# Performance work log

Hardware: AMD Instinct MI355X
Metric: run time of the kernel (lower is better)

The kernel has to match this reference:

```python
import jax, jax.numpy as jnp
import numpy as np

N = 50000
E = 800000
D = 128
L = 2


def setup_inputs() -> dict:
    key = jax.random.key(0)
    ks = jax.random.split(key, 8)
    x = jax.random.normal(ks[0], (N, D), dtype=jnp.float32)
    edge_index = jax.random.randint(ks[1], (2, E), 0, N, dtype=jnp.int64)
    s = 1.0 / np.sqrt(D)
    Wl = jax.random.uniform(ks[2], (L, D, D), jnp.float32, -s, s)  # neighbor transform (with bias)
    bl = jax.random.uniform(ks[3], (L, D), jnp.float32, -s, s)
    Wr = jax.random.uniform(ks[4], (L, D, D), jnp.float32, -s, s)  # root/self transform (no bias)
    W = jax.random.uniform(ks[5], (D, D), jnp.float32, -s, s)      # final Linear
    b = jax.random.uniform(ks[6], (D,), jnp.float32, -s, s)
    return {"x": x, "edge_index": edge_index, "Wl": Wl, "bl": bl, "Wr": Wr, "W": W, "b": b}


def reference(x, edge_index, Wl, bl, Wr, W, b):
    src, dst = edge_index[0], edge_index[1]
    n = x.shape[0]
    for l in range(Wl.shape[0]):
        # gather neighbor (source) features, scatter-max into destination nodes
        agg = jax.ops.segment_max(x[src], dst, num_segments=n)  # [N, D]
        agg = jnp.where(jnp.isneginf(agg), 0.0, agg)  # PyG: isolated nodes -> 0
        # SAGEConv: lin_l(agg) + lin_r(x)
        x = agg @ Wl[l].T + bl[l] + x @ Wr[l].T
        x = jax.nn.relu(x)
    return x @ W.T + b
```

## Files before the change

kernel.cpp:

```cpp
#include <hip/hip_runtime.h>
#include <math.h>

#define NN 50000
#define NE 800000
#define DD 128
#define NBUCK 196
#define PTILE 4096
#define PBLOCKS 196

typedef unsigned short u16;
typedef short s8v __attribute__((ext_vector_type(8)));
typedef float f16v __attribute__((ext_vector_type(16)));

__device__ __forceinline__ u16 f2bf(float f) {
    unsigned u = __float_as_uint(f);
    return (u16)((u + 0x7FFFu + ((u >> 16) & 1u)) >> 16);
}
__device__ __forceinline__ float bf2f(u16 h) {
    return __uint_as_float(((unsigned)h) << 16);
}
__device__ __forceinline__ float bflo(unsigned u) { return __uint_as_float(u << 16); }
__device__ __forceinline__ float bfhi(unsigned u) { return __uint_as_float(u & 0xFFFF0000u); }

__global__ __launch_bounds__(256) void zero_int(int* __restrict__ p, int n) {
    int i = blockIdx.x * 256 + threadIdx.x;
    if (i < n) p[i] = 0;
}

__global__ __launch_bounds__(256) void bucket_hist(const int* __restrict__ ei,
                                                   int* __restrict__ bcnt) {
    __shared__ int h[NBUCK];
    for (int i = threadIdx.x; i < NBUCK; i += 256) h[i] = 0;
    __syncthreads();
    int e0 = blockIdx.x * PTILE;
#pragma unroll
    for (int i = 0; i < 16; i++) {
        int e = e0 + i * 256 + threadIdx.x;
        if (e < NE) atomicAdd(&h[ei[NE + e] >> 8], 1);
    }
    __syncthreads();
    for (int i = threadIdx.x; i < NBUCK; i += 256)
        if (h[i]) atomicAdd(&bcnt[i], h[i]);
}

__global__ __launch_bounds__(256) void bucket_scan(const int* __restrict__ bcnt,
                                                   int* __restrict__ bbase,
                                                   int* __restrict__ bcur,
                                                   int* __restrict__ rowptr) {
    __shared__ int s[256];
    int t = threadIdx.x;
    int v = (t < NBUCK) ? bcnt[t] : 0;
    s[t] = v;
    __syncthreads();
    for (int o = 1; o < 256; o <<= 1) {
        int u = (t >= o) ? s[t - o] : 0;
        __syncthreads();
        s[t] += u;
        __syncthreads();
    }
    int ex = s[t] - v;
    if (t < NBUCK) { bbase[t] = ex; bcur[t] = ex; }
    if (t == 0) rowptr[NN] = NE;
}

__global__ __launch_bounds__(256) void bucket_partition(const int* __restrict__ ei,
                                                        int* __restrict__ bcur,
                                                        unsigned* __restrict__ packed) {
    __shared__ int h[NBUCK];
    __shared__ int base[NBUCK];
    int t = threadIdx.x;
    for (int i = t; i < NBUCK; i += 256) h[i] = 0;
    __syncthreads();
    int e0 = blockIdx.x * PTILE;
    int dsts[16], srcs[16];
#pragma unroll
    for (int i = 0; i < 16; i++) {
        int e = e0 + i * 256 + t;
        if (e < NE) {
            dsts[i] = ei[NE + e];
            srcs[i] = ei[e];
            atomicAdd(&h[dsts[i] >> 8], 1);
        } else dsts[i] = -1;
    }
    __syncthreads();
    for (int i = t; i < NBUCK; i += 256) {
        int c = h[i];
        base[i] = c ? atomicAdd(&bcur[i], c) : 0;
    }
    __syncthreads();
    for (int i = t; i < NBUCK; i += 256) h[i] = 0;
    __syncthreads();
#pragma unroll
    for (int i = 0; i < 16; i++) {
        if (dsts[i] >= 0) {
            int bk = dsts[i] >> 8;
            int r = atomicAdd(&h[bk], 1);
            packed[base[bk] + r] = (unsigned)srcs[i] | ((unsigned)(dsts[i] & 255) << 16);
        }
    }
}

__global__ __launch_bounds__(256) void bucket_csr(const unsigned* __restrict__ packed,
                                                  const int* __restrict__ bcnt,
                                                  const int* __restrict__ bbase,
                                                  int* __restrict__ rowptr,
                                                  int* __restrict__ col) {
    __shared__ int deg[256];
    __shared__ int off[256];
    int bk = blockIdx.x;
    int cnt = bcnt[bk], base = bbase[bk];
    int t = threadIdx.x;
    deg[t] = 0;
    __syncthreads();
    for (int i = t; i < cnt; i += 256) atomicAdd(&deg[packed[base + i] >> 16], 1);
    __syncthreads();
    int v = deg[t];
    off[t] = v;
    __syncthreads();
    for (int o = 1; o < 256; o <<= 1) {
        int u = (t >= o) ? off[t - o] : 0;
        __syncthreads();
        off[t] += u;
        __syncthreads();
    }
    int ex = off[t] - v;
    int node = (bk << 8) + t;
    if (node < NN) rowptr[node] = base + ex;
    deg[t] = ex;
    __syncthreads();
    for (int i = t; i < cnt; i += 256) {
        unsigned p = packed[base + i];
        int dl = p >> 16;
        int r = atomicAdd(&deg[dl], 1);
        col[base + r] = (int)(p & 0xFFFFu);
    }
}

__global__ __launch_bounds__(256) void conv_bf16(const float4* __restrict__ in,
                                                 ushort4* __restrict__ out, int n4) {
    int i = blockIdx.x * 256 + threadIdx.x;
    if (i >= n4) return;
    float4 v = in[i];
    ushort4 o;
    o.x = f2bf(v.x); o.y = f2bf(v.y); o.z = f2bf(v.z); o.w = f2bf(v.w);
    out[i] = o;
}

template<int NKC16, bool TWO>
__global__ __launch_bounds__(256) void pack_weights(const float* __restrict__ Wl,
                                                    const float* __restrict__ Wr,
                                                    u16* __restrict__ out) {
    int o = blockIdx.x * 256 + threadIdx.x;
    if (o >= NKC16 * 2048) return;
    int j = o & 7;
    int l = (o >> 3) & 63;
    int cn = o >> 9;
    int n = cn & 3;
    int c = cn >> 2;
    int colj = n * 32 + (l & 31);
    int k = c * 16 + (l >> 5) * 8 + j;
    float v;
    if (TWO) v = (k < DD) ? Wl[colj * DD + k] : Wr[colj * DD + (k - DD)];
    else     v = Wl[colj * DD + k];
    out[o] = f2bf(v);
}

__global__ __launch_bounds__(256) void agg_kernel_bf(const uint4* __restrict__ xb4,
                                                     const int* __restrict__ row_ptr,
                                                     const int* __restrict__ col,
                                                     uint4* __restrict__ aggb4) {
    int node = blockIdx.x * 16 + (threadIdx.x >> 4);
    if (node >= NN) return;
    int j = threadIdx.x & 15;
    int s0 = row_ptr[node], s1 = row_ptr[node + 1];
    if (s0 == s1) {
        aggb4[(size_t)node * 16 + j] = make_uint4(0, 0, 0, 0);
        return;
    }
    float m0[8], m1[8], m2[8], m3[8];
#pragma unroll
    for (int q = 0; q < 8; q++) { m0[q] = m1[q] = m2[q] = m3[q] = -INFINITY; }
    int i = s0;
    for (; i + 4 <= s1; i += 4) {
        int c0 = col[i], c1 = col[i + 1], c2 = col[i + 2], c3 = col[i + 3];
        uint4 v0 = xb4[(size_t)c0 * 16 + j];
        uint4 v1 = xb4[(size_t)c1 * 16 + j];
        uint4 v2 = xb4[(size_t)c2 * 16 + j];
        uint4 v3 = xb4[(size_t)c3 * 16 + j];
        m0[0] = fmaxf(m0[0], bflo(v0.x)); m0[1] = fmaxf(m0[1], bfhi(v0.x));
        m0[2] = fmaxf(m0[2], bflo(v0.y)); m0[3] = fmaxf(m0[3], bfhi(v0.y));
        m0[4] = fmaxf(m0[4], bflo(v0.z)); m0[5] = fmaxf(m0[5], bfhi(v0.z));
        m0[6] = fmaxf(m0[6], bflo(v0.w)); m0[7] = fmaxf(m0[7], bfhi(v0.w));
        m1[0] = fmaxf(m1[0], bflo(v1.x)); m1[1] = fmaxf(m1[1], bfhi(v1.x));
        m1[2] = fmaxf(m1[2], bflo(v1.y)); m1[3] = fmaxf(m1[3], bfhi(v1.y));
        m1[4] = fmaxf(m1[4], bflo(v1.z)); m1[5] = fmaxf(m1[5], bfhi(v1.z));
        m1[6] = fmaxf(m1[6], bflo(v1.w)); m1[7] = fmaxf(m1[7], bfhi(v1.w));
        m2[0] = fmaxf(m2[0], bflo(v2.x)); m2[1] = fmaxf(m2[1], bfhi(v2.x));
        m2[2] = fmaxf(m2[2], bflo(v2.y)); m2[3] = fmaxf(m2[3], bfhi(v2.y));
        m2[4] = fmaxf(m2[4], bflo(v2.z)); m2[5] = fmaxf(m2[5], bfhi(v2.z));
        m2[6] = fmaxf(m2[6], bflo(v2.w)); m2[7] = fmaxf(m2[7], bfhi(v2.w));
        m3[0] = fmaxf(m3[0], bflo(v3.x)); m3[1] = fmaxf(m3[1], bfhi(v3.x));
        m3[2] = fmaxf(m3[2], bflo(v3.y)); m3[3] = fmaxf(m3[3], bfhi(v3.y));
        m3[4] = fmaxf(m3[4], bflo(v3.z)); m3[5] = fmaxf(m3[5], bfhi(v3.z));
        m3[6] = fmaxf(m3[6], bflo(v3.w)); m3[7] = fmaxf(m3[7], bfhi(v3.w));
    }
    for (; i < s1; i++) {
        uint4 v = xb4[(size_t)col[i] * 16 + j];
        m0[0] = fmaxf(m0[0], bflo(v.x)); m0[1] = fmaxf(m0[1], bfhi(v.x));
        m0[2] = fmaxf(m0[2], bflo(v.y)); m0[3] = fmaxf(m0[3], bfhi(v.y));
        m0[4] = fmaxf(m0[4], bflo(v.z)); m0[5] = fmaxf(m0[5], bfhi(v.z));
        m0[6] = fmaxf(m0[6], bflo(v.w)); m0[7] = fmaxf(m0[7], bfhi(v.w));
    }
#pragma unroll
    for (int q = 0; q < 8; q++) m0[q] = fmaxf(fmaxf(m0[q], m1[q]), fmaxf(m2[q], m3[q]));
    uint4 o;
    o.x = (__float_as_uint(m0[0]) >> 16) | (__float_as_uint(m0[1]) & 0xFFFF0000u);
    o.y = (__float_as_uint(m0[2]) >> 16) | (__float_as_uint(m0[3]) & 0xFFFF0000u);
    o.z = (__float_as_uint(m0[4]) >> 16) | (__float_as_uint(m0[5]) & 0xFFFF0000u);
    o.w = (__float_as_uint(m0[6]) >> 16) | (__float_as_uint(m0[7]) & 0xFFFF0000u);
    aggb4[(size_t)node * 16 + j] = o;
}

template<int NKC16, bool TWO_SRC, bool RELU, bool OUT_BF16>
__global__ __launch_bounds__(256) void mfma_gemm(const u16* __restrict__ srcA,
                                                 const u16* __restrict__ srcB,
                                                 const u16* __restrict__ Bpk,
                                                 const float* __restrict__ bias,
                                                 void* __restrict__ outv) {
    __shared__ s8v ldsB[NKC16 * 4 * 64];
    int tid = threadIdx.x;
#pragma unroll
    for (int i = 0; i < NKC16; i++) {
        ((float4*)ldsB)[tid + 256 * i] = ((const float4*)Bpk)[tid + 256 * i];
    }

    int wt = tid >> 6;
    int lane = tid & 63;
    int row0 = blockIdx.x * 128 + wt * 32;
    int rload = row0 + (lane & 31);
    if (rload > NN - 1) rload = NN - 1;
    int koff = (lane >> 5) * 8;

    f16v acc[4];
#pragma unroll
    for (int n = 0; n < 4; n++) acc[n] = (f16v)(0.0f);

    __syncthreads();

#pragma unroll
    for (int c = 0; c < NKC16; c++) {
        const u16* s = srcA;
        int kk = c * 16;
        if (TWO_SRC && c >= 8) { s = srcB; kk = (c - 8) * 16; }
        s8v a = *(const s8v*)(s + (size_t)rload * DD + kk + koff);
#pragma unroll
        for (int n = 0; n < 4; n++) {
            s8v b = ldsB[(c * 4 + n) * 64 + lane];
            acc[n] = __builtin_amdgcn_mfma_f32_32x32x16_bf16(a, b, acc[n], 0, 0, 0);
        }
    }

    int rowadd = 4 * (lane >> 5);
#pragma unroll
    for (int n = 0; n < 4; n++) {
        int colj = n * 32 + (lane & 31);
        float bj = bias[colj];
#pragma unroll
        for (int r = 0; r < 16; r++) {
            int row = row0 + (r & 3) + 8 * (r >> 2) + rowadd;
            if (row < NN) {
                float v = acc[n][r] + bj;
                if (RELU) v = fmaxf(v, 0.0f);
                if (OUT_BF16) ((u16*)outv)[(size_t)row * DD + colj] = f2bf(v);
                else          ((float*)outv)[(size_t)row * DD + colj] = v;
            }
        }
    }
}

extern "C" void kernel_launch(void* const* d_in, const int* in_sizes, int n_in,
                              void* d_out, int out_size, void* d_ws, size_t ws_size,
                              hipStream_t stream) {
    const float* x  = (const float*)d_in[0];
    const int*   ei = (const int*)d_in[1];
    const float* Wl = (const float*)d_in[2];
    const float* bl = (const float*)d_in[3];
    const float* Wr = (const float*)d_in[4];
    const float* W  = (const float*)d_in[5];
    const float* b  = (const float*)d_in[6];
    float* out = (float*)d_out;

    u16* aggb = (u16*)d_ws;
    u16* hb0  = aggb + (size_t)NN * DD;
    u16* hb1  = hb0 + (size_t)NN * DD;
    u16* Bpk0 = hb1 + (size_t)NN * DD;
    u16* Bpk1 = Bpk0 + 32768;
    u16* Bpkf = Bpk1 + 32768;
    unsigned* packed = (unsigned*)(Bpkf + 16384);
    int* col    = (int*)(packed + NE);
    int* rowptr = col + NE;
    int* bcnt   = rowptr + NN + 1;
    int* bbase  = bcnt + NBUCK;
    int* bcur   = bbase + NBUCK;

    dim3 blk(256);
    int gemmBlocks = (NN + 127) / 128;
    int aggBlocks  = (NN + 15) / 16;
    int convBlocks = (NN * DD / 4 + 255) / 256;

    zero_int<<<1, blk, 0, stream>>>(bcnt, NBUCK);
    bucket_hist<<<PBLOCKS, blk, 0, stream>>>(ei, bcnt);
    bucket_scan<<<1, blk, 0, stream>>>(bcnt, bbase, bcur, rowptr);
    bucket_partition<<<PBLOCKS, blk, 0, stream>>>(ei, bcur, packed);
    bucket_csr<<<NBUCK, blk, 0, stream>>>(packed, bcnt, bbase, rowptr, col);

    conv_bf16<<<convBlocks, blk, 0, stream>>>((const float4*)x, (ushort4*)hb0, NN * DD / 4);
    pack_weights<16, true><<<128, blk, 0, stream>>>(Wl, Wr, Bpk0);
    pack_weights<16, true><<<128, blk, 0, stream>>>(Wl + DD * DD, Wr + DD * DD, Bpk1);
    pack_weights<8, false><<<64, blk, 0, stream>>>(W, nullptr, Bpkf);

    agg_kernel_bf<<<aggBlocks, blk, 0, stream>>>((const uint4*)hb0, rowptr, col, (uint4*)aggb);
    mfma_gemm<16, true, true, true><<<gemmBlocks, blk, 0, stream>>>(
        aggb, hb0, Bpk0, bl, hb1);

    agg_kernel_bf<<<aggBlocks, blk, 0, stream>>>((const uint4*)hb1, rowptr, col, (uint4*)aggb);
    mfma_gemm<16, true, true, true><<<gemmBlocks, blk, 0, stream>>>(
        aggb, hb1, Bpk1, bl + DD, hb0);

    mfma_gemm<8, false, false, false><<<gemmBlocks, blk, 0, stream>>>(
        hb0, nullptr, Bpkf, b, out);
}
```

Before: 245.6 us.

## Fuse prep kernels, unroll gather by 8, read GEMM weights directly from global

Merges the zeroing, x-to-bf16 conversion and three weight-packing launches into one prep kernel that dispatches on block index, cutting four kernel launches. The aggregation loop adds an 8-wide unrolled stage so more neighbor gathers are in flight per thread. The GEMM drops the LDS staging of packed weights and its barrier, loading B fragments straight from global/L2 instead. That trades LDS setup cost for repeated global reads of the weights by every block.

```diff
diff --git a/kernel.cpp b/kernel.cpp
--- a/kernel.cpp
+++ b/kernel.cpp
@@ -7,6 +7,7 @@
 #define NBUCK 196
 #define PTILE 4096
 #define PBLOCKS 196
+#define CONVB 6250
 
 typedef unsigned short u16;
 typedef short s8v __attribute__((ext_vector_type(8)));
@@ -16,15 +17,48 @@
     unsigned u = __float_as_uint(f);
     return (u16)((u + 0x7FFFu + ((u >> 16) & 1u)) >> 16);
 }
-__device__ __forceinline__ float bf2f(u16 h) {
-    return __uint_as_float(((unsigned)h) << 16);
-}
 __device__ __forceinline__ float bflo(unsigned u) { return __uint_as_float(u << 16); }
 __device__ __forceinline__ float bfhi(unsigned u) { return __uint_as_float(u & 0xFFFF0000u); }
 
-__global__ __launch_bounds__(256) void zero_int(int* __restrict__ p, int n) {
-    int i = blockIdx.x * 256 + threadIdx.x;
-    if (i < n) p[i] = 0;
+__device__ __forceinline__ void pack_one(const float* __restrict__ Wl,
+                                         const float* __restrict__ Wr,
+                                         bool two, int o, u16* __restrict__ out) {
+    int j = o & 7;
+    int l = (o >> 3) & 63;
+    int cn = o >> 9;
+    int n = cn & 3;
+    int c = cn >> 2;
+    int colj = n * 32 + (l & 31);
+    int k = c * 16 + (l >> 5) * 8 + j;
+    float v;
+    if (two) v = (k < DD) ? Wl[colj * DD + k] : Wr[colj * DD + (k - DD)];
+    else     v = Wl[colj * DD + k];
+    out[o] = f2bf(v);
+}
+
+__global__ __launch_bounds__(256) void prep_kernel(
+        const float4* __restrict__ x4, ushort4* __restrict__ hb0,
+        const float* __restrict__ Wl, const float* __restrict__ Wr,
+        const float* __restrict__ W,
+        u16* __restrict__ Bpk0, u16* __restrict__ Bpk1, u16* __restrict__ Bpkf,
+        int* __restrict__ bcnt) {
+    int bid = blockIdx.x;
+    int tid = threadIdx.x;
+    if (bid < CONVB) {
+        int i = bid * 256 + tid;
+        float4 v = x4[i];
+        ushort4 o;
+        o.x = f2bf(v.x); o.y = f2bf(v.y); o.z = f2bf(v.z); o.w = f2bf(v.w);
+        hb0[i] = o;
+    } else if (bid < CONVB + 128) {
+        pack_one(Wl, Wr, true, (bid - CONVB) * 256 + tid, Bpk0);
+    } else if (bid < CONVB + 256) {
+        pack_one(Wl + DD * DD, Wr + DD * DD, true, (bid - CONVB - 128) * 256 + tid, Bpk1);
+    } else if (bid < CONVB + 320) {
+        pack_one(W, W, false, (bid - CONVB - 256) * 256 + tid, Bpkf);
+    } else {
+        if (tid < NBUCK) bcnt[tid] = 0;
+    }
 }
 
 __global__ __launch_bounds__(256) void bucket_hist(const int* __restrict__ ei,
@@ -136,33 +170,11 @@
     }
 }
 
-__global__ __launch_bounds__(256) void conv_bf16(const float4* __restrict__ in,
-                                                 ushort4* __restrict__ out, int n4) {
-    int i = blockIdx.x * 256 + threadIdx.x;
-    if (i >= n4) return;
-    float4 v = in[i];
-    ushort4 o;
-    o.x = f2bf(v.x); o.y = f2bf(v.y); o.z = f2bf(v.z); o.w = f2bf(v.w);
-    out[i] = o;
-}
-
-template<int NKC16, bool TWO>
-__global__ __launch_bounds__(256) void pack_weights(const float* __restrict__ Wl,
-                                                    const float* __restrict__ Wr,
-                                                    u16* __restrict__ out) {
-    int o = blockIdx.x * 256 + threadIdx.x;
-    if (o >= NKC16 * 2048) return;
-    int j = o & 7;
-    int l = (o >> 3) & 63;
-    int cn = o >> 9;
-    int n = cn & 3;
-    int c = cn >> 2;
-    int colj = n * 32 + (l & 31);
-    int k = c * 16 + (l >> 5) * 8 + j;
-    float v;
-    if (TWO) v = (k < DD) ? Wl[colj * DD + k] : Wr[colj * DD + (k - DD)];
-    else     v = Wl[colj * DD + k];
-    out[o] = f2bf(v);
+__device__ __forceinline__ void vmax8(float* m, uint4 v) {
+    m[0] = fmaxf(m[0], bflo(v.x)); m[1] = fmaxf(m[1], bfhi(v.x));
+    m[2] = fmaxf(m[2], bflo(v.y)); m[3] = fmaxf(m[3], bfhi(v.y));
+    m[4] = fmaxf(m[4], bflo(v.z)); m[5] = fmaxf(m[5], bfhi(v.z));
+    m[6] = fmaxf(m[6], bflo(v.w)); m[7] = fmaxf(m[7], bfhi(v.w));
 }
 
 __global__ __launch_bounds__(256) void agg_kernel_bf(const uint4* __restrict__ xb4,
@@ -181,35 +193,31 @@
 #pragma unroll
     for (int q = 0; q < 8; q++) { m0[q] = m1[q] = m2[q] = m3[q] = -INFINITY; }
     int i = s0;
+    for (; i + 8 <= s1; i += 8) {
+        int c0 = col[i],     c1 = col[i + 1], c2 = col[i + 2], c3 = col[i + 3];
+        int c4 = col[i + 4], c5 = col[i + 5], c6 = col[i + 6], c7 = col[i + 7];
+        uint4 v0 = xb4[(size_t)c0 * 16 + j];
+        uint4 v1 = xb4[(size_t)c1 * 16 + j];
+        uint4 v2 = xb4[(size_t)c2 * 16 + j];
+        uint4 v3 = xb4[(size_t)c3 * 16 + j];
+        uint4 v4 = xb4[(size_t)c4 * 16 + j];
+        uint4 v5 = xb4[(size_t)c5 * 16 + j];
+        uint4 v6 = xb4[(size_t)c6 * 16 + j];
+        uint4 v7 = xb4[(size_t)c7 * 16 + j];
+        vmax8(m0, v0); vmax8(m1, v1); vmax8(m2, v2); vmax8(m3, v3);
+        vmax8(m0, v4); vmax8(m1, v5); vmax8(m2, v6); vmax8(m3, v7);
+    }
     for (; i + 4 <= s1; i += 4) {
         int c0 = col[i], c1 = col[i + 1], c2 = col[i + 2], c3 = col[i + 3];
         uint4 v0 = xb4[(size_t)c0 * 16 + j];
         uint4 v1 = xb4[(size_t)c1 * 16 + j];
         uint4 v2 = xb4[(size_t)c2 * 16 + j];
         uint4 v3 = xb4[(size_t)c3 * 16 + j];
-        m0[0] = fmaxf(m0[0], bflo(v0.x)); m0[1] = fmaxf(m0[1], bfhi(v0.x));
-        m0[2] = fmaxf(m0[2], bflo(v0.y)); m0[3] = fmaxf(m0[3], bfhi(v0.y));
-        m0[4] = fmaxf(m0[4], bflo(v0.z)); m0[5] = fmaxf(m0[5], bfhi(v0.z));
-        m0[6] = fmaxf(m0[6], bflo(v0.w)); m0[7] = fmaxf(m0[7], bfhi(v0.w));
-        m1[0] = fmaxf(m1[0], bflo(v1.x)); m1[1] = fmaxf(m1[1], bfhi(v1.x));
-        m1[2] = fmaxf(m1[2], bflo(v1.y)); m1[3] = fmaxf(m1[3], bfhi(v1.y));
-        m1[4] = fmaxf(m1[4], bflo(v1.z)); m1[5] = fmaxf(m1[5], bfhi(v1.z));
-        m1[6] = fmaxf(m1[6], bflo(v1.w)); m1[7] = fmaxf(m1[7], bfhi(v1.w));
-        m2[0] = fmaxf(m2[0], bflo(v2.x)); m2[1] = fmaxf(m2[1], bfhi(v2.x));
-        m2[2] = fmaxf(m2[2], bflo(v2.y)); m2[3] = fmaxf(m2[3], bfhi(v2.y));
-        m2[4] = fmaxf(m2[4], bflo(v2.z)); m2[5] = fmaxf(m2[5], bfhi(v2.z));
-        m2[6] = fmaxf(m2[6], bflo(v2.w)); m2[7] = fmaxf(m2[7], bfhi(v2.w));
-        m3[0] = fmaxf(m3[0], bflo(v3.x)); m3[1] = fmaxf(m3[1], bfhi(v3.x));
-        m3[2] = fmaxf(m3[2], bflo(v3.y)); m3[3] = fmaxf(m3[3], bfhi(v3.y));
-        m3[4] = fmaxf(m3[4], bflo(v3.z)); m3[5] = fmaxf(m3[5], bfhi(v3.z));
-        m3[6] = fmaxf(m3[6], bflo(v3.w)); m3[7] = fmaxf(m3[7], bfhi(v3.w));
+        vmax8(m0, v0); vmax8(m1, v1); vmax8(m2, v2); vmax8(m3, v3);
     }
     for (; i < s1; i++) {
         uint4 v = xb4[(size_t)col[i] * 16 + j];
-        m0[0] = fmaxf(m0[0], bflo(v.x)); m0[1] = fmaxf(m0[1], bfhi(v.x));
-        m0[2] = fmaxf(m0[2], bflo(v.y)); m0[3] = fmaxf(m0[3], bfhi(v.y));
-        m0[4] = fmaxf(m0[4], bflo(v.z)); m0[5] = fmaxf(m0[5], bfhi(v.z));
-        m0[6] = fmaxf(m0[6], bflo(v.w)); m0[7] = fmaxf(m0[7], bfhi(v.w));
+        vmax8(m0, v);
     }
 #pragma unroll
     for (int q = 0; q < 8; q++) m0[q] = fmaxf(fmaxf(m0[q], m1[q]), fmaxf(m2[q], m3[q]));
@@ -227,25 +235,18 @@
                                                  const u16* __restrict__ Bpk,
                                                  const float* __restrict__ bias,
                                                  void* __restrict__ outv) {
-    __shared__ s8v ldsB[NKC16 * 4 * 64];
     int tid = threadIdx.x;
-#pragma unroll
-    for (int i = 0; i < NKC16; i++) {
-        ((float4*)ldsB)[tid + 256 * i] = ((const float4*)Bpk)[tid + 256 * i];
-    }
-
     int wt = tid >> 6;
     int lane = tid & 63;
     int row0 = blockIdx.x * 128 + wt * 32;
     int rload = row0 + (lane & 31);
     if (rload > NN - 1) rload = NN - 1;
     int koff = (lane >> 5) * 8;
+    const s8v* Bv = (const s8v*)Bpk;
 
     f16v acc[4];
 #pragma unroll
     for (int n = 0; n < 4; n++) acc[n] = (f16v)(0.0f);
-
-    __syncthreads();
 
 #pragma unroll
     for (int c = 0; c < NKC16; c++) {
@@ -255,7 +256,7 @@
         s8v a = *(const s8v*)(s + (size_t)rload * DD + kk + koff);
 #pragma unroll
         for (int n = 0; n < 4; n++) {
-            s8v b = ldsB[(c * 4 + n) * 64 + lane];
+            s8v b = Bv[(c * 4 + n) * 64 + lane];
             acc[n] = __builtin_amdgcn_mfma_f32_32x32x16_bf16(a, b, acc[n], 0, 0, 0);
         }
     }
@@ -306,19 +307,16 @@
     dim3 blk(256);
     int gemmBlocks = (NN + 127) / 128;
     int aggBlocks  = (NN + 15) / 16;
-    int convBlocks = (NN * DD / 4 + 255) / 256;
-
-    zero_int<<<1, blk, 0, stream>>>(bcnt, NBUCK);
+    int prepBlocks = CONVB + 320 + 1;
+
+    prep_kernel<<<prepBlocks, blk, 0, stream>>>(
+        (const float4*)x, (ushort4*)hb0, Wl, Wr, W, Bpk0, Bpk1, Bpkf, bcnt);
+
     bucket_hist<<<PBLOCKS, blk, 0, stream>>>(ei, bcnt);
     bucket_scan<<<1, blk, 0, stream>>>(bcnt, bbase, bcur, rowptr);
     bucket_partition<<<PBLOCKS, blk, 0, stream>>>(ei, bcur, packed);
     bucket_csr<<<NBUCK, blk, 0, stream>>>(packed, bcnt, bbase, rowptr, col);
 
-    conv_bf16<<<convBlocks, blk, 0, stream>>>((const float4*)x, (ushort4*)hb0, NN * DD / 4);
-    pack_weights<16, true><<<128, blk, 0, stream>>>(Wl, Wr, Bpk0);
-    pack_weights<16, true><<<128, blk, 0, stream>>>(Wl + DD * DD, Wr + DD * DD, Bpk1);
-    pack_weights<8, false><<<64, blk, 0, stream>>>(W, nullptr, Bpkf);
-
     agg_kernel_bf<<<aggBlocks, blk, 0, stream>>>((const uint4*)hb0, rowptr, col, (uint4*)aggb);
     mfma_gemm<16, true, true, true><<<gemmBlocks, blk, 0, stream>>>(
         aggb, hb0, Bpk0, bl, hb1);
```

Result: no change. 241.6 us (-1.6%).
